# Kernel tuning notes

Hardware: AMD Instinct MI355X
Metric: run time of the kernel (lower is better)

## Reference

```python
import jax, jax.numpy as jnp
import numpy as np

N = 170000      # nodes
E = 2400000     # edges
F_IN = 128      # dataset.num_features
H = 64          # hidden_channels
C = 40          # dataset.num_classes
L = 8           # num_layers
ENTROPY = 1.0   # args.entropy
EPS = 1e-20


def setup_inputs() -> dict:
    key = jax.random.key(0)
    ks = jax.random.split(key, 10)
    x = jax.random.normal(ks[0], (N, F_IN), jnp.float32)
    edge_src = jax.random.randint(ks[1], (E,), 0, N)
    edge_dst = jax.random.randint(ks[2], (E,), 0, N)
    edge_weight = jax.random.uniform(ks[3], (E,), jnp.float32) / 14.0  # ~1/deg scale
    u = jax.random.uniform(ks[4], (N, L + 1), jnp.float32, 1e-6, 1.0 - 1e-6)
    gumbel = -jnp.log(-jnp.log(u))  # standard Gumbel noise for gumbel_softmax
    lin0_w = jax.random.normal(ks[5], (F_IN, H), jnp.float32) / np.float32(np.sqrt(F_IN))
    lin0_b = jnp.zeros((H,), jnp.float32)
    meta_w = jax.random.normal(ks[6], (H, 1), jnp.float32) / np.float32(np.sqrt(H))
    meta_b = jnp.zeros((1,), jnp.float32)
    lin1_w = jax.random.normal(ks[7], (H, C), jnp.float32) / np.float32(np.sqrt(H))
    lin1_b = jnp.zeros((C,), jnp.float32)
    return dict(x=x, edge_weight=edge_weight, gumbel=gumbel,
                lin0_w=lin0_w, lin0_b=lin0_b, meta_w=meta_w, meta_b=meta_b,
                lin1_w=lin1_w, lin1_b=lin1_b,
                edge_src=edge_src, edge_dst=edge_dst)


def reference(x, edge_weight, gumbel, lin0_w, lin0_b, meta_w, meta_b,
              lin1_w, lin1_b, edge_src, edge_dst):
    # input projection + relu (dropout=0 -> no-op)
    x = jnp.maximum(x @ lin0_w + lin0_b, 0.0)  # [N,H]
    xs = [x]
    # GCNII layers with conv.alpha = conv.beta = 0 -> pure edge-weighted
    # scatter-add propagation followed by relu.
    for _ in range(L):
        msg = edge_weight[:, None] * x[edge_src]              # [E,H] gather
        x = jax.ops.segment_sum(msg, edge_dst, num_segments=N)  # [N,H] scatter-add
        x = jnp.maximum(x, 0.0)
        xs.append(x)
    xMat = jnp.stack(xs, axis=1)  # [N, L+1, H] (preds == xMatrix since concat='none')
    # MetaNet: [N, L+1]
    r = jnp.squeeze(xMat @ meta_w, -1) + meta_b[0]
    # get_t: stick-breaking with sigmoid; last column uses t=1 times cumprod
    s = jax.nn.sigmoid(r)                                    # [N, L+1]
    cp_excl = jnp.concatenate(
        [jnp.ones((N, 1), s.dtype), jnp.cumprod(1.0 - s, axis=1)[:, :-1]], axis=1)
    t = s * cp_excl
    t = t.at[:, -1].set(cp_excl[:, -1])
    ent_loss = ENTROPY * (-(jnp.log(t + EPS) * t).sum(1).mean())
    # gumbel_softmax(log(t+eps), tau=1, hard=False)
    tM = jax.nn.softmax(jnp.log(t + EPS) + gumbel, axis=1)   # [N, L+1]
    # layer mixing: [N,1,L+1] @ [N,L+1,H] -> [N,H]
    out = jnp.einsum('nl,nlh->nh', tM, xMat)
    out = out @ lin1_w + lin1_b
    return jax.nn.log_softmax(out, axis=-1), ent_loss
```

## Files before the change

### kernel.cpp

```cpp
#include <hip/hip_runtime.h>
#include <hip/hip_bf16.h>

#define N_NODES 170000
#define N_EDGES 2400000
#define F_IN_   128
#define H_      64
#define C_OUT   40
#define L_LAYERS 8
#define LP1     9
#define EPS_T   1e-20f
#define ROW_ELEMS (LP1 * H_)

typedef unsigned short u16;
typedef unsigned short u16x8 __attribute__((ext_vector_type(8)));
typedef short bf16x8 __attribute__((ext_vector_type(8)));
typedef float f32x4 __attribute__((ext_vector_type(4)));

__device__ __forceinline__ float bf2f(u16 u) {
    union { unsigned int i; float f; } c; c.i = ((unsigned int)u) << 16; return c.f;
}
__device__ __forceinline__ u16 f2bf(float f) {
    __hip_bfloat16 h = __float2bfloat16(f);
    return *reinterpret_cast<u16*>(&h);
}

__device__ __forceinline__ float waveReduceSum(float v) {
    for (int m = 32; m; m >>= 1) v += __shfl_xor(v, m, 64);
    return v;
}
__device__ __forceinline__ float waveReduceMax(float v) {
    for (int m = 32; m; m >>= 1) v = fmaxf(v, __shfl_xor(v, m, 64));
    return v;
}

__global__ __launch_bounds__(256) void k_zero4(float4* __restrict__ p) {
    p[blockIdx.x * 256 + threadIdx.x] = make_float4(0.f, 0.f, 0.f, 0.f);
}

__global__ __launch_bounds__(256) void k_hist(
    const int* __restrict__ edst, int* __restrict__ deg)
{
    int e = blockIdx.x * 256 + threadIdx.x;
    if (e < N_EDGES) atomicAdd(&deg[edst[e]], 1);
}

#define SCAN_TPB 256
#define SCAN_VPT 8
#define SCAN_EPB (SCAN_TPB * SCAN_VPT)
#define SCAN_BLOCKS ((N_NODES + SCAN_EPB - 1) / SCAN_EPB)

__global__ __launch_bounds__(SCAN_TPB) void k_scan1(
    const int* __restrict__ deg, int* __restrict__ rowstart,
    int* __restrict__ blockSums)
{
    __shared__ int tsum[SCAN_TPB];
    int tid = threadIdx.x;
    int base = blockIdx.x * SCAN_EPB + tid * SCAN_VPT;
    int vals[SCAN_VPT];
    int local = 0;
    #pragma unroll
    for (int i = 0; i < SCAN_VPT; ++i) {
        int idx = base + i;
        int v = (idx < N_NODES) ? deg[idx] : 0;
        vals[i] = local;
        local += v;
    }
    tsum[tid] = local;
    __syncthreads();
    for (int off = 1; off < SCAN_TPB; off <<= 1) {
        int v = (tid >= off) ? tsum[tid - off] : 0;
        __syncthreads();
        tsum[tid] += v;
        __syncthreads();
    }
    int texcl = tsum[tid] - local;
    #pragma unroll
    for (int i = 0; i < SCAN_VPT; ++i) {
        int idx = base + i;
        if (idx < N_NODES) rowstart[idx] = texcl + vals[i];
    }
    if (tid == SCAN_TPB - 1) blockSums[blockIdx.x] = tsum[tid];
}

__global__ __launch_bounds__(64) void k_scan2(int* __restrict__ blockSums) {
    if (threadIdx.x == 0) {
        int acc = 0;
        for (int i = 0; i < SCAN_BLOCKS; ++i) {
            int v = blockSums[i];
            blockSums[i] = acc;
            acc += v;
        }
    }
}

__global__ __launch_bounds__(SCAN_TPB) void k_scan3(
    int* __restrict__ rowstart, const int* __restrict__ blockSums)
{
    int off = blockSums[blockIdx.x];
    int base = blockIdx.x * SCAN_EPB + threadIdx.x * SCAN_VPT;
    #pragma unroll
    for (int i = 0; i < SCAN_VPT; ++i) {
        int idx = base + i;
        if (idx < N_NODES) rowstart[idx] += off;
    }
}

__global__ __launch_bounds__(256) void k_bucket(
    const int* __restrict__ esrc, const int* __restrict__ edst,
    const float* __restrict__ ew, const int* __restrict__ rowstart,
    int* __restrict__ cursor, int2* __restrict__ csr, int lo, int hi)
{
    int e = blockIdx.x * 256 + threadIdx.x;
    if (e >= N_EDGES) return;
    int d = edst[e];
    if (d < lo || d >= hi) return;
    int p = rowstart[d] + atomicAdd(&cursor[d], 1);
    csr[p] = make_int2(esrc[e], __float_as_int(ew[e]));
}

__global__ __launch_bounds__(256) void k_lin0(
    const float* __restrict__ x, const float* __restrict__ W0,
    const float* __restrict__ b0, const float* __restrict__ mw,
    const float* __restrict__ mb, u16* __restrict__ xMatB,
    float* __restrict__ r)
{
    __shared__ u16 Wt[H_ * F_IN_];
    int tid = threadIdx.x;
    for (int i = tid; i < F_IN_ * H_; i += 256) {
        int k = i >> 6, c = i & 63;
        Wt[c * F_IN_ + (k ^ ((c & 7) << 3))] = f2bf(W0[i]);
    }
    __syncthreads();

    int wave = tid >> 6, lane = tid & 63;
    int lg = lane >> 4;
    int lr = lane & 15;

    bf16x8 bfrag[4][4];
    float b0v[4], mwv[4];
    #pragma unroll
    for (int ct = 0; ct < 4; ++ct) {
        int c = ct * 16 + lr;
        #pragma unroll
        for (int kt = 0; kt < 4; ++kt) {
            int kidx = (kt * 32 + lg * 8) ^ ((c & 7) << 3);
            bfrag[ct][kt] = *reinterpret_cast<bf16x8*>(&Wt[c * F_IN_ + kidx]);
        }
        b0v[ct] = b0[c];
        mwv[ct] = mw[c];
    }
    float mb0 = mb[0];

    int nbase = blockIdx.x * 256 + wave * 64;
    #pragma unroll
    for (int m = 0; m < 4; ++m) {
        int arow = nbase + m * 16 + lr;
        int arowc = (arow < N_NODES) ? arow : (N_NODES - 1);
        const float4* xrow = (const float4*)(x + (size_t)arowc * F_IN_);
        f32x4 acc[4];
        #pragma unroll
        for (int ct = 0; ct < 4; ++ct) {
            acc[ct][0] = b0v[ct]; acc[ct][1] = b0v[ct];
            acc[ct][2] = b0v[ct]; acc[ct][3] = b0v[ct];
        }
        #pragma unroll
        for (int kt = 0; kt < 4; ++kt) {
            int k8 = kt * 8 + lg * 2;
            float4 xa = xrow[k8];
            float4 xb = xrow[k8 + 1];
            bf16x8 a;
            a[0] = (short)f2bf(xa.x); a[1] = (short)f2bf(xa.y);
            a[2] = (short)f2bf(xa.z); a[3] = (short)f2bf(xa.w);
            a[4] = (short)f2bf(xb.x); a[5] = (short)f2bf(xb.y);
            a[6] = (short)f2bf(xb.z); a[7] = (short)f2bf(xb.w);
            #pragma unroll
            for (int ct = 0; ct < 4; ++ct)
                acc[ct] = __builtin_amdgcn_mfma_f32_16x16x32_bf16(
                    a, bfrag[ct][kt], acc[ct], 0, 0, 0);
        }
        float p[4];
        #pragma unroll
        for (int reg = 0; reg < 4; ++reg) {
            int n = nbase + m * 16 + lg * 4 + reg;
            float pr = 0.f;
            #pragma unroll
            for (int ct = 0; ct < 4; ++ct) {
                float v = fmaxf(acc[ct][reg], 0.f);
                if (n < N_NODES)
                    xMatB[(size_t)n * ROW_ELEMS + ct * 16 + lr] = f2bf(v);
                pr = fmaf(v, mwv[ct], pr);
            }
            p[reg] = pr;
        }
        #pragma unroll
        for (int reg = 0; reg < 4; ++reg) {
            p[reg] += __shfl_xor(p[reg], 1, 64);
            p[reg] += __shfl_xor(p[reg], 2, 64);
            p[reg] += __shfl_xor(p[reg], 4, 64);
            p[reg] += __shfl_xor(p[reg], 8, 64);
        }
        if (lr < 4) {
            int n = nbase + m * 16 + lg * 4 + lr;
            if (n < N_NODES) r[n * LP1] = p[lr] + mb0;
        }
    }
}

__global__ __launch_bounds__(256) void k_prop(
    const u16* __restrict__ xMatB, int l,
    const int* __restrict__ rowstart, const int* __restrict__ deg,
    const int2* __restrict__ csr,
    const float* __restrict__ mw, const float* __restrict__ mb,
    u16* __restrict__ xMatOut, float* __restrict__ r)
{
    int tid = threadIdx.x;
    int oc = tid & 7;
    int n = blockIdx.x * 32 + (tid >> 3);
    bool valid = (n < N_NODES);
    int start = valid ? rowstart[n] : 0;
    int d     = valid ? deg[n]      : 0;

    const unsigned loff = (unsigned)l * H_ + oc * 8;
    float acc0[8] = {0.f,0.f,0.f,0.f,0.f,0.f,0.f,0.f};
    float acc1[8] = {0.f,0.f,0.f,0.f,0.f,0.f,0.f,0.f};

    int t = 0;
    while (__any(t < d)) {
        if (t < d) {
            int2 e = csr[start + t];
            float w = __int_as_float(e.y);
            u16x8 v = *reinterpret_cast<const u16x8*>(
                &xMatB[(size_t)(unsigned)e.x * ROW_ELEMS + loff]);
            #pragma unroll
            for (int j = 0; j < 8; ++j) acc0[j] = fmaf(bf2f(v[j]), w, acc0[j]);
        }
        if (t + 1 < d) {
            int2 e = csr[start + t + 1];
            float w = __int_as_float(e.y);
            u16x8 v = *reinterpret_cast<const u16x8*>(
                &xMatB[(size_t)(unsigned)e.x * ROW_ELEMS + loff]);
            #pragma unroll
            for (int j = 0; j < 8; ++j) acc1[j] = fmaf(bf2f(v[j]), w, acc1[j]);
        }
        t += 2;
    }

    float a[8];
    #pragma unroll
    for (int j = 0; j < 8; ++j) a[j] = fmaxf(acc0[j] + acc1[j], 0.f);

    if (valid) {
        u16x8 o;
        #pragma unroll
        for (int j = 0; j < 8; ++j) o[j] = f2bf(a[j]);
        *reinterpret_cast<u16x8*>(
            &xMatOut[(size_t)n * ROW_ELEMS + (l + 1) * H_ + oc * 8]) = o;
    }
    float dot = 0.f;
    #pragma unroll
    for (int j = 0; j < 8; ++j) dot = fmaf(a[j], mw[oc * 8 + j], dot);
    dot += __shfl_xor(dot, 1, 64);
    dot += __shfl_xor(dot, 2, 64);
    dot += __shfl_xor(dot, 4, 64);
    if (valid && oc == 0) r[n * LP1 + (l + 1)] = dot + mb[0];
}

__global__ __launch_bounds__(256) void k_gate(
    const float* __restrict__ r, const float* __restrict__ gum,
    float* __restrict__ tM, float* __restrict__ entPart)
{
    __shared__ float lds[4];
    int tid = threadIdx.x;
    int n = blockIdx.x * 256 + tid;
    float ent = 0.f;
    if (n < N_NODES) {
        float t[LP1], lg[LP1];
        float cp = 1.f;
        #pragma unroll
        for (int j = 0; j < LP1; ++j) {
            float rv = r[n * LP1 + j];
            float s = 1.f / (1.f + expf(-rv));
            t[j] = (j == L_LAYERS) ? cp : s * cp;
            cp *= (1.f - s);
        }
        float mx = -INFINITY;
        #pragma unroll
        for (int j = 0; j < LP1; ++j) {
            float lt = logf(t[j] + EPS_T);
            ent -= t[j] * lt;
            lg[j] = lt + gum[n * LP1 + j];
            mx = fmaxf(mx, lg[j]);
        }
        float se = 0.f;
        #pragma unroll
        for (int j = 0; j < LP1; ++j) { lg[j] = expf(lg[j] - mx); se += lg[j]; }
        float inv = 1.f / se;
        #pragma unroll
        for (int j = 0; j < LP1; ++j) tM[n * LP1 + j] = lg[j] * inv;
    }
    float s = waveReduceSum(ent);
    int wave = tid >> 6, lane = tid & 63;
    if (lane == 0) lds[wave] = s;
    __syncthreads();
    if (tid == 0) entPart[blockIdx.x] = lds[0] + lds[1] + lds[2] + lds[3];
}

__global__ __launch_bounds__(256) void k_final(
    const u16* __restrict__ xMatB, const float* __restrict__ tM,
    const float* __restrict__ W1, const float* __restrict__ b1,
    float* __restrict__ out)
{
    __shared__ float mixLds[4][H_];
    int tid = threadIdx.x, wave = tid >> 6, lane = tid & 63;
    int n = blockIdx.x * 4 + wave;
    float tm = (lane < LP1) ? tM[n * LP1 + lane] : 0.f;
    float m = 0.f;
    #pragma unroll
    for (int j = 0; j < LP1; ++j) {
        float w = __shfl(tm, j, 64);
        m = fmaf(w, bf2f(xMatB[(size_t)n * ROW_ELEMS + j * H_ + lane]), m);
    }
    mixLds[wave][lane] = m;
    __syncthreads();
    float o = -INFINITY;
    if (lane < C_OUT) {
        float a = b1[lane];
        #pragma unroll 8
        for (int h = 0; h < H_; ++h)
            a = fmaf(mixLds[wave][h], W1[h * C_OUT + lane], a);
        o = a;
    }
    float omx = waveReduceMax(o);
    float ex = (lane < C_OUT) ? expf(o - omx) : 0.f;
    float es = waveReduceSum(ex);
    if (lane < C_OUT)
        out[(size_t)n * C_OUT + lane] = o - omx - logf(es);
}

__global__ __launch_bounds__(256) void k_entreduce(
    const float* __restrict__ part, int n, float scale, float* __restrict__ out)
{
    __shared__ float lds[4];
    int tid = threadIdx.x;
    float s = 0.f;
    for (int i = tid; i < n; i += 256) s += part[i];
    s = waveReduceSum(s);
    int wave = tid >> 6, lane = tid & 63;
    if (lane == 0) lds[wave] = s;
    __syncthreads();
    if (tid == 0) out[0] = (lds[0] + lds[1] + lds[2] + lds[3]) * scale;
}

extern "C" void kernel_launch(void* const* d_in, const int* in_sizes, int n_in,
                              void* d_out, int out_size, void* d_ws, size_t ws_size,
                              hipStream_t stream)
{
    const float* x   = (const float*)d_in[0];
    const float* ew  = (const float*)d_in[1];
    const float* gum = (const float*)d_in[2];
    const float* W0  = (const float*)d_in[3];
    const float* b0  = (const float*)d_in[4];
    const float* mw  = (const float*)d_in[5];
    const float* mb  = (const float*)d_in[6];
    const float* W1  = (const float*)d_in[7];
    const float* b1  = (const float*)d_in[8];
    const int* esrc  = (const int*)d_in[9];
    const int* edst  = (const int*)d_in[10];
    float* out = (float*)d_out;

    const size_t xMatBytes = (size_t)N_NODES * ROW_ELEMS * sizeof(u16);
    const size_t rBytes    = (size_t)N_NODES * LP1 * sizeof(float);
    const size_t tMBytes   = (size_t)N_NODES * LP1 * sizeof(float);
    const size_t entBytes  = (size_t)((N_NODES + 255) / 256) * sizeof(float);
    const size_t degBytes  = (size_t)N_NODES * sizeof(int);
    const size_t curBytes  = (size_t)N_NODES * sizeof(int);
    const size_t rowBytes  = (size_t)N_NODES * sizeof(int);
    const size_t bsBytes   = 512;
    const size_t csrBytes  = (size_t)N_EDGES * sizeof(int2);
    const size_t need = xMatBytes + rBytes + tMBytes + entBytes + degBytes +
                        curBytes + rowBytes + bsBytes + csrBytes;
    if (ws_size < need) return;

    char* p = (char*)d_ws;
    u16*  xMatB    = (u16*)p;           p += xMatBytes;
    float* rbuf    = (float*)p;         p += rBytes;
    float* tMbuf   = (float*)p;         p += tMBytes;
    float* entP    = (float*)p;         p += entBytes;
    int*  deg      = (int*)p;           p += degBytes;
    int*  cursor   = (int*)p;           p += curBytes;
    int*  rowstart = (int*)p;           p += rowBytes;
    int*  blockSums= (int*)p;           p += bsBytes;
    int2* csr      = (int2*)p;

    const int nodeBlocks = N_NODES / 4;
    const int edgeBlocks = (N_EDGES + 255) / 256;
    const int gateBlocks = (N_NODES + 255) / 256;
    const int lin0Blocks = (N_NODES + 255) / 256;
    const int propBlocks = (N_NODES + 31) / 32;

    k_zero4<<<333, 256, 0, stream>>>((float4*)deg);
    k_hist<<<edgeBlocks, 256, 0, stream>>>(edst, deg);
    k_scan1<<<SCAN_BLOCKS, SCAN_TPB, 0, stream>>>(deg, rowstart, blockSums);
    k_scan2<<<1, 64, 0, stream>>>(blockSums);
    k_scan3<<<SCAN_BLOCKS, SCAN_TPB, 0, stream>>>(rowstart, blockSums);
    const int STEP = N_NODES / 8;
    for (int i = 0; i < 8; ++i)
        k_bucket<<<edgeBlocks, 256, 0, stream>>>(esrc, edst, ew, rowstart,
                                                 cursor, csr, i * STEP,
                                                 (i + 1) * STEP);

    k_lin0<<<lin0Blocks, 256, 0, stream>>>(x, W0, b0, mw, mb, xMatB, rbuf);
    for (int l = 0; l < L_LAYERS; ++l)
        k_prop<<<propBlocks, 256, 0, stream>>>(xMatB, l, rowstart, deg, csr,
                                               mw, mb, xMatB, rbuf);
    k_gate<<<gateBlocks, 256, 0, stream>>>(rbuf, gum, tMbuf, entP);
    k_final<<<nodeBlocks, 256, 0, stream>>>(xMatB, tMbuf, W1, b1, out);
    k_entreduce<<<1, 256, 0, stream>>>(entP, gateBlocks, 1.0f / N_NODES,
                                       out + (size_t)N_NODES * C_OUT);
}
```

Baseline: 885.1 us.

## Split final stage into vectorized layer-mix and MFMA-based lin1 with log-softmax

The per-node final kernel, which used one wave per node with scalar loads and a serial 64-term dot product per class, is replaced by two kernels. A mix kernel has 8 threads per node, each doing 16-byte vector loads of the bf16 layer rows, and writes the mixed features in bf16 to a buffer that overlays the rbuf/CSR workspace. A lin1 kernel stages a swizzled bf16 copy of W1 in LDS and uses 16x16x32 bf16 MFMA to compute the logits, followed by a shuffle-based log-softmax. This adds an extra round trip of the mixed features through global memory and rounds both the mix and W1 to bf16.

New measurement: 841.5 us. -4.9%, faster.

```diff
diff --git a/kernel.cpp b/kernel.cpp
--- a/kernel.cpp
+++ b/kernel.cpp
@@ -26,10 +26,6 @@
 
 __device__ __forceinline__ float waveReduceSum(float v) {
     for (int m = 32; m; m >>= 1) v += __shfl_xor(v, m, 64);
-    return v;
-}
-__device__ __forceinline__ float waveReduceMax(float v) {
-    for (int m = 32; m; m >>= 1) v = fmaxf(v, __shfl_xor(v, m, 64));
     return v;
 }
 
@@ -305,36 +301,99 @@
     if (tid == 0) entPart[blockIdx.x] = lds[0] + lds[1] + lds[2] + lds[3];
 }
 
-__global__ __launch_bounds__(256) void k_final(
+__global__ __launch_bounds__(256) void k_mix(
     const u16* __restrict__ xMatB, const float* __restrict__ tM,
-    const float* __restrict__ W1, const float* __restrict__ b1,
-    float* __restrict__ out)
-{
-    __shared__ float mixLds[4][H_];
-    int tid = threadIdx.x, wave = tid >> 6, lane = tid & 63;
-    int n = blockIdx.x * 4 + wave;
-    float tm = (lane < LP1) ? tM[n * LP1 + lane] : 0.f;
-    float m = 0.f;
+    u16* __restrict__ mix)
+{
+    int t = blockIdx.x * 256 + threadIdx.x;
+    int n = t >> 3, oc = t & 7;
+    if (n >= N_NODES) return;
+    const u16* row = &xMatB[(size_t)n * ROW_ELEMS + oc * 8];
+    const float* tMn = &tM[n * LP1];
+    float acc[8] = {0.f,0.f,0.f,0.f,0.f,0.f,0.f,0.f};
     #pragma unroll
     for (int j = 0; j < LP1; ++j) {
-        float w = __shfl(tm, j, 64);
-        m = fmaf(w, bf2f(xMatB[(size_t)n * ROW_ELEMS + j * H_ + lane]), m);
-    }
-    mixLds[wave][lane] = m;
+        u16x8 v = *reinterpret_cast<const u16x8*>(&row[j * H_]);
+        float w = tMn[j];
+        #pragma unroll
+        for (int q = 0; q < 8; ++q) acc[q] = fmaf(bf2f(v[q]), w, acc[q]);
+    }
+    u16x8 o;
+    #pragma unroll
+    for (int q = 0; q < 8; ++q) o[q] = f2bf(acc[q]);
+    *reinterpret_cast<u16x8*>(&mix[(size_t)n * H_ + oc * 8]) = o;
+}
+
+__global__ __launch_bounds__(256) void k_lin1(
+    const u16* __restrict__ mix, const float* __restrict__ W1,
+    const float* __restrict__ b1, float* __restrict__ out)
+{
+    __shared__ u16 Wl[48 * 64];
+    int tid = threadIdx.x;
+    for (int i = tid; i < 48 * 64; i += 256) {
+        int c = i >> 6, k = i & 63;
+        float v = (c < C_OUT) ? W1[k * C_OUT + c] : 0.f;
+        Wl[c * 64 + (k ^ ((c & 7) << 3))] = f2bf(v);
+    }
     __syncthreads();
-    float o = -INFINITY;
-    if (lane < C_OUT) {
-        float a = b1[lane];
-        #pragma unroll 8
-        for (int h = 0; h < H_; ++h)
-            a = fmaf(mixLds[wave][h], W1[h * C_OUT + lane], a);
-        o = a;
-    }
-    float omx = waveReduceMax(o);
-    float ex = (lane < C_OUT) ? expf(o - omx) : 0.f;
-    float es = waveReduceSum(ex);
-    if (lane < C_OUT)
-        out[(size_t)n * C_OUT + lane] = o - omx - logf(es);
+
+    int wave = tid >> 6, lane = tid & 63;
+    int lg = lane >> 4, lr = lane & 15;
+
+    bf16x8 bfrag[3][2];
+    float b1v[3];
+    #pragma unroll
+    for (int ct = 0; ct < 3; ++ct) {
+        int c = ct * 16 + lr;
+        #pragma unroll
+        for (int kt = 0; kt < 2; ++kt) {
+            int kidx = (kt * 32 + lg * 8) ^ ((c & 7) << 3);
+            bfrag[ct][kt] = *reinterpret_cast<bf16x8*>(&Wl[c * 64 + kidx]);
+        }
+        b1v[ct] = (c < C_OUT) ? b1[c] : 0.f;
+    }
+
+    int nbase = blockIdx.x * 64 + wave * 16;
+    int arow = nbase + lr;
+    int arowc = (arow < N_NODES) ? arow : (N_NODES - 1);
+    const u16* mrow = &mix[(size_t)arowc * H_];
+
+    f32x4 acc[3];
+    #pragma unroll
+    for (int ct = 0; ct < 3; ++ct) {
+        acc[ct][0] = b1v[ct]; acc[ct][1] = b1v[ct];
+        acc[ct][2] = b1v[ct]; acc[ct][3] = b1v[ct];
+    }
+    #pragma unroll
+    for (int kt = 0; kt < 2; ++kt) {
+        bf16x8 a = *reinterpret_cast<const bf16x8*>(&mrow[kt * 32 + lg * 8]);
+        #pragma unroll
+        for (int ct = 0; ct < 3; ++ct)
+            acc[ct] = __builtin_amdgcn_mfma_f32_16x16x32_bf16(
+                a, bfrag[ct][kt], acc[ct], 0, 0, 0);
+    }
+    #pragma unroll
+    for (int reg = 0; reg < 4; ++reg) {
+        float v0 = acc[0][reg], v1 = acc[1][reg];
+        float v2 = (lr < 8) ? acc[2][reg] : -INFINITY;
+        float mx = fmaxf(fmaxf(v0, v1), v2);
+        mx = fmaxf(mx, __shfl_xor(mx, 1, 64));
+        mx = fmaxf(mx, __shfl_xor(mx, 2, 64));
+        mx = fmaxf(mx, __shfl_xor(mx, 4, 64));
+        mx = fmaxf(mx, __shfl_xor(mx, 8, 64));
+        float e = expf(v0 - mx) + expf(v1 - mx) + ((lr < 8) ? expf(v2 - mx) : 0.f);
+        e += __shfl_xor(e, 1, 64);
+        e += __shfl_xor(e, 2, 64);
+        e += __shfl_xor(e, 4, 64);
+        e += __shfl_xor(e, 8, 64);
+        float ls = mx + logf(e);
+        int n = nbase + lg * 4 + reg;
+        if (n < N_NODES) {
+            out[(size_t)n * C_OUT + lr]      = v0 - ls;
+            out[(size_t)n * C_OUT + 16 + lr] = v1 - ls;
+            if (lr < 8) out[(size_t)n * C_OUT + 32 + lr] = v2 - ls;
+        }
+    }
 }
 
 __global__ __launch_bounds__(256) void k_entreduce(
@@ -369,34 +428,38 @@
     float* out = (float*)d_out;
 
     const size_t xMatBytes = (size_t)N_NODES * ROW_ELEMS * sizeof(u16);
-    const size_t rBytes    = (size_t)N_NODES * LP1 * sizeof(float);
     const size_t tMBytes   = (size_t)N_NODES * LP1 * sizeof(float);
     const size_t entBytes  = (size_t)((N_NODES + 255) / 256) * sizeof(float);
+    const size_t rBytes    = (size_t)N_NODES * LP1 * sizeof(float);
     const size_t degBytes  = (size_t)N_NODES * sizeof(int);
     const size_t curBytes  = (size_t)N_NODES * sizeof(int);
     const size_t rowBytes  = (size_t)N_NODES * sizeof(int);
     const size_t bsBytes   = 512;
     const size_t csrBytes  = (size_t)N_EDGES * sizeof(int2);
-    const size_t need = xMatBytes + rBytes + tMBytes + entBytes + degBytes +
+    const size_t mixBytes  = (size_t)N_NODES * H_ * sizeof(u16);
+    const size_t need = xMatBytes + tMBytes + entBytes + rBytes + degBytes +
                         curBytes + rowBytes + bsBytes + csrBytes;
     if (ws_size < need) return;
 
     char* p = (char*)d_ws;
     u16*  xMatB    = (u16*)p;           p += xMatBytes;
-    float* rbuf    = (float*)p;         p += rBytes;
     float* tMbuf   = (float*)p;         p += tMBytes;
     float* entP    = (float*)p;         p += entBytes;
+    char* overlay  = p;
+    float* rbuf    = (float*)p;         p += rBytes;
     int*  deg      = (int*)p;           p += degBytes;
     int*  cursor   = (int*)p;           p += curBytes;
     int*  rowstart = (int*)p;           p += rowBytes;
     int*  blockSums= (int*)p;           p += bsBytes;
     int2* csr      = (int2*)p;
-
-    const int nodeBlocks = N_NODES / 4;
+    u16*  mixbuf   = (u16*)overlay;
+
     const int edgeBlocks = (N_EDGES + 255) / 256;
     const int gateBlocks = (N_NODES + 255) / 256;
     const int lin0Blocks = (N_NODES + 255) / 256;
     const int propBlocks = (N_NODES + 31) / 32;
+    const int mixBlocks  = (N_NODES * 8 + 255) / 256;
+    const int lin1Blocks = (N_NODES + 63) / 64;
 
     k_zero4<<<333, 256, 0, stream>>>((float4*)deg);
     k_hist<<<edgeBlocks, 256, 0, stream>>>(edst, deg);
@@ -414,7 +477,8 @@
         k_prop<<<propBlocks, 256, 0, stream>>>(xMatB, l, rowstart, deg, csr,
                                                mw, mb, xMatB, rbuf);
     k_gate<<<gateBlocks, 256, 0, stream>>>(rbuf, gum, tMbuf, entP);
-    k_final<<<nodeBlocks, 256, 0, stream>>>(xMatB, tMbuf, W1, b1, out);
+    k_mix<<<mixBlocks, 256, 0, stream>>>(xMatB, tMbuf, mixbuf);
+    k_lin1<<<lin1Blocks, 256, 0, stream>>>(mixbuf, W1, b1, out);
     k_entreduce<<<1, 256, 0, stream>>>(entP, gateBlocks, 1.0f / N_NODES,
                                        out + (size_t)N_NODES * C_OUT);
 }
```
